# Kernel tuning notes

Hardware: AMD Instinct MI355X
Metric: run time of the kernel (lower is better)

Reference implementation:

```python
import jax, jax.numpy as jnp
import numpy as np

N_NODES = 100000
N_EDGES = 1600000
HIDDEN = 128
IN_CH = 128


def setup_inputs() -> dict:
    key = jax.random.key(0)
    ks = jax.random.split(key, 7)
    x = jax.random.normal(ks[0], (N_NODES, IN_CH), dtype=jnp.float32)
    # edge_index with no self-loops (col != row), matching remove_self_loops
    row = jax.random.randint(ks[1], (N_EDGES,), 0, N_NODES)
    off = jax.random.randint(ks[2], (N_EDGES,), 1, N_NODES)
    col = (row + off) % N_NODES
    edge_index = jnp.stack([row, col], axis=0).astype(jnp.int64)
    Wi = jax.random.normal(ks[3], (HIDDEN, IN_CH), dtype=jnp.float32) * (1.0 / np.sqrt(IN_CH))
    bi = jax.random.normal(ks[4], (HIDDEN,), dtype=jnp.float32) * 0.01
    A = jax.random.normal(ks[5], (HIDDEN, HIDDEN), dtype=jnp.float32) * (1.0 / np.sqrt(HIDDEN))
    Wp = jax.random.normal(ks[6], (HIDDEN, HIDDEN + 2), dtype=jnp.float32) * (1.0 / np.sqrt(HIDDEN))
    return {"x": x, "edge_index": edge_index, "Wi": Wi, "bi": bi, "A": A,
            "Wp": Wp, "num_layers": 4}


def _pairwise_weight(Wp):
    # W0: strictly-upper part symmetrized; diag = q * row-abs-sum + r
    W0 = jnp.triu(Wp[:, :-2], 1)
    W0 = W0 + W0.T
    q = Wp[:, -2]
    r = Wp[:, -1]
    return W0 + jnp.diag(q * jnp.sum(jnp.abs(W0), axis=1) + r)


def reference(x, edge_index, Wi, bi, A, Wp, num_layers):
    n = x.shape[0]
    row, col = edge_index[0], edge_index[1]
    # degree-based symmetric normalization (degree of target nodes)
    deg = jax.ops.segment_sum(jnp.ones_like(col, dtype=x.dtype), col, num_segments=n)
    dinv = jnp.where(deg > 0, jax.lax.rsqrt(jnp.maximum(deg, 1.0)), 0.0)
    norm = dinv[row] * dinv[col]  # [edges]

    Weff = _pairwise_weight(Wp)          # symmetric [H, H]
    Asym = A - A.T                       # antisymmetric [H, H]

    h = jax.nn.relu(x @ Wi.T + bi)       # input projection (dropout eval = id)
    for _ in range(num_layers):
        out = h @ Weff.T                 # symmetric aggr pre-mix
        msg = norm[:, None] * out[row]   # gather + per-edge scale [E, H]
        agg = jax.ops.segment_sum(msg, col, num_segments=n)  # scatter-add
        delta = agg - jax.nn.relu(h @ Asym.T)
        h = h + jax.nn.relu(jnp.tanh(delta))
    return h
```

## Files before the change

kernel.cpp:

```cpp
#include <hip/hip_runtime.h>
#include <hip/hip_bf16.h>

#define HID 128
#define NLAYERS 4
#define SCHUNK 2048
#define WSHIFT 13

typedef __attribute__((ext_vector_type(8))) short bf16x8;
typedef __attribute__((ext_vector_type(4))) float f32x4;

__device__ __forceinline__ float bf2f(unsigned short u) {
    union { unsigned int i; float f; } v; v.i = ((unsigned int)u) << 16; return v.f;
}
__device__ __forceinline__ unsigned short f2bf(float f) {
    union { float f; unsigned int i; } v; v.f = f;
    unsigned int r = v.i + 0x7FFF + ((v.i >> 16) & 1);
    return (unsigned short)(r >> 16);
}

__global__ void k_detect(const unsigned int* ei, int* flag) {
    __shared__ int s;
    if (threadIdx.x == 0) s = 1;
    __syncthreads();
    unsigned int w = ei[threadIdx.x * 2 + 1];
    if (w != 0) s = 0;
    __syncthreads();
    if (threadIdx.x == 0) *flag = s;
}

__global__ void k_convert_edges(const void* ei, const int* flag, int* row32, int* col32,
                                int* deg, int ne) {
    int e = blockIdx.x * blockDim.x + threadIdx.x;
    if (e >= ne) return;
    int r, c;
    if (*flag) {
        const long long* p = (const long long*)ei;
        r = (int)p[e];
        c = (int)p[(size_t)ne + e];
    } else {
        const int* p = (const int*)ei;
        r = p[e];
        c = p[(size_t)ne + e];
    }
    row32[e] = r;
    col32[e] = c;
    atomicAdd(&deg[c], 1);
}

__global__ void k_scan1(const int* deg, int* partial, float* dinv, int n) {
    int tid = threadIdx.x, lane = tid & 63, wid = tid >> 6;
    int i0 = blockIdx.x * SCHUNK + tid * 8;
    int ts = 0;
    #pragma unroll
    for (int j = 0; j < 8; ++j) {
        int i = i0 + j;
        if (i < n) {
            int d = deg[i];
            ts += d;
            dinv[i] = (d > 0) ? rsqrtf((float)d) : 0.f;
        }
    }
    #pragma unroll
    for (int m = 1; m < 64; m <<= 1) ts += __shfl_xor(ts, m);
    __shared__ int ws[4];
    if (lane == 0) ws[wid] = ts;
    __syncthreads();
    if (tid == 0) partial[blockIdx.x] = ws[0] + ws[1] + ws[2] + ws[3];
}

__global__ void k_scan2(int* partial, int nb) {
    int tid = threadIdx.x;
    int v = (tid < nb) ? partial[tid] : 0;
    int s = v;
    #pragma unroll
    for (int off = 1; off < 64; off <<= 1) {
        int t = __shfl_up(s, off);
        if (tid >= off) s += t;
    }
    if (tid < nb) partial[tid] = s - v;
}

__global__ void k_scan3(const int* deg, const int* partial, int* offs, int* pos, int n, int ne) {
    int tid = threadIdx.x, lane = tid & 63, wid = tid >> 6;
    int i0 = blockIdx.x * SCHUNK + tid * 8;
    int v[8], ts = 0;
    #pragma unroll
    for (int j = 0; j < 8; ++j) { v[j] = (i0 + j < n) ? deg[i0 + j] : 0; ts += v[j]; }
    int s = ts;
    #pragma unroll
    for (int off = 1; off < 64; off <<= 1) { int t = __shfl_up(s, off); if (lane >= off) s += t; }
    __shared__ int ws[4];
    if (lane == 63) ws[wid] = s;
    __syncthreads();
    int run = partial[blockIdx.x] + (s - ts);
    for (int w = 0; w < wid; ++w) run += ws[w];
    #pragma unroll
    for (int j = 0; j < 8; ++j) {
        if (i0 + j < n) { offs[i0 + j] = run; pos[i0 + j] = run; }
        run += v[j];
    }
    if (blockIdx.x == 0 && tid == 0) offs[n] = ne;
}

__global__ void k_csrfill(const int* row32, const int* col32, int* pos, int* csr,
                          int ne, int nwin) {
    int cls = blockIdx.x & 7;
    int slice = blockIdx.x >> 3;
    int e0 = (slice * blockDim.x + threadIdx.x) * 4;
    int r[4], c[4], w[4];
    #pragma unroll
    for (int k = 0; k < 4; ++k) {
        int e = e0 + k;
        if (e < ne) { c[k] = col32[e]; r[k] = row32[e]; w[k] = c[k] >> WSHIFT; }
        else w[k] = -1;
    }
    for (int p = cls; p < nwin; p += 8) {
        #pragma unroll
        for (int k = 0; k < 4; ++k) {
            if (w[k] == p) {
                int q = atomicAdd(&pos[c[k]], 1);
                csr[q] = r[k];
            }
        }
    }
}

__global__ void k_weff(const float* Wp, unsigned short* WeffB) {
    int i = blockIdx.x, j = threadIdx.x;
    float w = (i < j) ? Wp[i * 130 + j] : ((i > j) ? Wp[j * 130 + i] : 0.f);
    float a = fabsf(w);
    #pragma unroll
    for (int m = 1; m < 64; m <<= 1) a += __shfl_xor(a, m);
    __shared__ float ws[2];
    if ((j & 63) == 0) ws[j >> 6] = a;
    __syncthreads();
    float rs = ws[0] + ws[1];
    if (i == j) w = Wp[i * 130 + 128] * rs + Wp[i * 130 + 129];
    WeffB[i * 128 + j] = f2bf(w);
}

__global__ void k_asym_wi(const float* A, const float* Wi, unsigned short* AsymB, unsigned short* WiB) {
    int idx = blockIdx.x * blockDim.x + threadIdx.x;
    if (idx >= 16384) return;
    int i = idx >> 7, j = idx & 127;
    AsymB[idx] = f2bf(A[idx] - A[j * 128 + i]);
    WiB[idx] = f2bf(Wi[idx]);
}

__launch_bounds__(256, 2)
__global__ void k_gemm0(const float* x, const unsigned short* WiB, const float* bi,
                        const float* dinv, float* h, unsigned short* hsb, int n) {
    int wid = threadIdx.x >> 6, lane = threadIdx.x & 63;
    int row0 = blockIdx.x * 64 + wid * 16;
    int lrow = lane & 15, lk = (lane >> 4) * 8;
    int arow = row0 + lrow; if (arow >= n) arow = n - 1;
    const float* Aptr = x + (size_t)arow * 128;
    f32x4 acc[8];
    #pragma unroll
    for (int cf = 0; cf < 8; ++cf) acc[cf] = (f32x4)(0.f);
    #pragma unroll
    for (int kk = 0; kk < 4; ++kk) {
        float4 xa = *(const float4*)(Aptr + kk * 32 + lk);
        float4 xc = *(const float4*)(Aptr + kk * 32 + lk + 4);
        bf16x8 a;
        a[0] = (short)f2bf(xa.x); a[1] = (short)f2bf(xa.y);
        a[2] = (short)f2bf(xa.z); a[3] = (short)f2bf(xa.w);
        a[4] = (short)f2bf(xc.x); a[5] = (short)f2bf(xc.y);
        a[6] = (short)f2bf(xc.z); a[7] = (short)f2bf(xc.w);
        #pragma unroll
        for (int cf = 0; cf < 8; ++cf) {
            bf16x8 b = *(const bf16x8*)(WiB + (size_t)(cf * 16 + lrow) * 128 + kk * 32 + lk);
            acc[cf] = __builtin_amdgcn_mfma_f32_16x16x32_bf16(a, b, acc[cf], 0, 0, 0);
        }
    }
    int orow_base = row0 + (lane >> 4) * 4;
    #pragma unroll
    for (int r = 0; r < 4; ++r) {
        int orow = orow_base + r;
        if (orow >= n) continue;
        float dv = dinv[orow];
        #pragma unroll
        for (int cf = 0; cf < 8; ++cf) {
            int col = cf * 16 + lrow;
            float v = acc[cf][r] + bi[col];
            v = fmaxf(v, 0.f);
            h[(size_t)orow * 128 + col] = v;
            hsb[(size_t)orow * 128 + col] = f2bf(v * dv);
        }
    }
}

__launch_bounds__(256, 8)
__global__ void k_gather(const unsigned short* hsb, const int* csr, const int* offs,
                         unsigned short* aggHb, int n) {
    int wid = threadIdx.x >> 6, lane = threadIdx.x & 63;
    int c = blockIdx.x * 4 + wid;
    if (c >= n) return;
    int g = lane >> 4;
    int fl = lane & 15;
    int s = offs[c], e = offs[c + 1];
    float accA[8], accB[8];
    #pragma unroll
    for (int k = 0; k < 8; ++k) { accA[k] = 0.f; accB[k] = 0.f; }
    int j = s;
    for (; j + 16 <= e; j += 16) {
        int r0 = csr[j + g];
        int r1 = csr[j + 4 + g];
        int r2 = csr[j + 8 + g];
        int r3 = csr[j + 12 + g];
        uint4 v0 = *(const uint4*)(hsb + (size_t)r0 * 128 + fl * 8);
        uint4 v1 = *(const uint4*)(hsb + (size_t)r1 * 128 + fl * 8);
        uint4 v2 = *(const uint4*)(hsb + (size_t)r2 * 128 + fl * 8);
        uint4 v3 = *(const uint4*)(hsb + (size_t)r3 * 128 + fl * 8);
        accA[0] += bf2f((unsigned short)(v0.x & 0xffff)); accA[1] += bf2f((unsigned short)(v0.x >> 16));
        accA[2] += bf2f((unsigned short)(v0.y & 0xffff)); accA[3] += bf2f((unsigned short)(v0.y >> 16));
        accA[4] += bf2f((unsigned short)(v0.z & 0xffff)); accA[5] += bf2f((unsigned short)(v0.z >> 16));
        accA[6] += bf2f((unsigned short)(v0.w & 0xffff)); accA[7] += bf2f((unsigned short)(v0.w >> 16));
        accB[0] += bf2f((unsigned short)(v1.x & 0xffff)); accB[1] += bf2f((unsigned short)(v1.x >> 16));
        accB[2] += bf2f((unsigned short)(v1.y & 0xffff)); accB[3] += bf2f((unsigned short)(v1.y >> 16));
        accB[4] += bf2f((unsigned short)(v1.z & 0xffff)); accB[5] += bf2f((unsigned short)(v1.z >> 16));
        accB[6] += bf2f((unsigned short)(v1.w & 0xffff)); accB[7] += bf2f((unsigned short)(v1.w >> 16));
        accA[0] += bf2f((unsigned short)(v2.x & 0xffff)); accA[1] += bf2f((unsigned short)(v2.x >> 16));
        accA[2] += bf2f((unsigned short)(v2.y & 0xffff)); accA[3] += bf2f((unsigned short)(v2.y >> 16));
        accA[4] += bf2f((unsigned short)(v2.z & 0xffff)); accA[5] += bf2f((unsigned short)(v2.z >> 16));
        accA[6] += bf2f((unsigned short)(v2.w & 0xffff)); accA[7] += bf2f((unsigned short)(v2.w >> 16));
        accB[0] += bf2f((unsigned short)(v3.x & 0xffff)); accB[1] += bf2f((unsigned short)(v3.x >> 16));
        accB[2] += bf2f((unsigned short)(v3.y & 0xffff)); accB[3] += bf2f((unsigned short)(v3.y >> 16));
        accB[4] += bf2f((unsigned short)(v3.z & 0xffff)); accB[5] += bf2f((unsigned short)(v3.z >> 16));
        accB[6] += bf2f((unsigned short)(v3.w & 0xffff)); accB[7] += bf2f((unsigned short)(v3.w >> 16));
    }
    for (; j < e; j += 8) {
        int i0 = j + g, i1 = j + 4 + g;
        if (i0 < e) {
            int r = csr[i0];
            uint4 v = *(const uint4*)(hsb + (size_t)r * 128 + fl * 8);
            accA[0] += bf2f((unsigned short)(v.x & 0xffff)); accA[1] += bf2f((unsigned short)(v.x >> 16));
            accA[2] += bf2f((unsigned short)(v.y & 0xffff)); accA[3] += bf2f((unsigned short)(v.y >> 16));
            accA[4] += bf2f((unsigned short)(v.z & 0xffff)); accA[5] += bf2f((unsigned short)(v.z >> 16));
            accA[6] += bf2f((unsigned short)(v.w & 0xffff)); accA[7] += bf2f((unsigned short)(v.w >> 16));
        }
        if (i1 < e) {
            int r = csr[i1];
            uint4 v = *(const uint4*)(hsb + (size_t)r * 128 + fl * 8);
            accB[0] += bf2f((unsigned short)(v.x & 0xffff)); accB[1] += bf2f((unsigned short)(v.x >> 16));
            accB[2] += bf2f((unsigned short)(v.y & 0xffff)); accB[3] += bf2f((unsigned short)(v.y >> 16));
            accB[4] += bf2f((unsigned short)(v.z & 0xffff)); accB[5] += bf2f((unsigned short)(v.z >> 16));
            accB[6] += bf2f((unsigned short)(v.w & 0xffff)); accB[7] += bf2f((unsigned short)(v.w >> 16));
        }
    }
    #pragma unroll
    for (int k = 0; k < 8; ++k) {
        float a = accA[k] + accB[k];
        a += __shfl_xor(a, 16);
        a += __shfl_xor(a, 32);
        accA[k] = a;
    }
    int f0 = fl * 8 + g * 2;
    unsigned int o = ((unsigned int)f2bf(accA[g * 2 + 1]) << 16) | (unsigned int)f2bf(accA[g * 2]);
    *(unsigned int*)(aggHb + (size_t)c * 128 + f0) = o;
}

__launch_bounds__(256, 8)
__global__ void k_gemm_upd(const unsigned short* aggHb, const unsigned short* WeffB,
                           const unsigned short* AsymB, const float* dinv,
                           float* h, unsigned short* hsb, int n) {
    __shared__ float zl[32][132];
    int wv = threadIdx.x >> 6, lane = threadIdx.x & 63;
    int t = wv & 1;
    int m = wv >> 1;
    int row0 = blockIdx.x * 32 + t * 16;
    int lrow = lane & 15, lk = (lane >> 4) * 8;
    int arow = row0 + lrow; if (arow >= n) arow = n - 1;
    f32x4 acc[8];
    #pragma unroll
    for (int cf = 0; cf < 8; ++cf) acc[cf] = (f32x4)(0.f);
    if (m == 1) {
        const float* Ap = h + (size_t)arow * 128;
        #pragma unroll
        for (int kk = 0; kk < 4; ++kk) {
            float4 xa = *(const float4*)(Ap + kk * 32 + lk);
            float4 xc = *(const float4*)(Ap + kk * 32 + lk + 4);
            bf16x8 a;
            a[0] = (short)f2bf(xa.x); a[1] = (short)f2bf(xa.y);
            a[2] = (short)f2bf(xa.z); a[3] = (short)f2bf(xa.w);
            a[4] = (short)f2bf(xc.x); a[5] = (short)f2bf(xc.y);
            a[6] = (short)f2bf(xc.z); a[7] = (short)f2bf(xc.w);
            #pragma unroll
            for (int cf = 0; cf < 8; ++cf) {
                bf16x8 b = *(const bf16x8*)(AsymB + (size_t)(cf * 16 + lrow) * 128 + kk * 32 + lk);
                acc[cf] = __builtin_amdgcn_mfma_f32_16x16x32_bf16(a, b, acc[cf], 0, 0, 0);
            }
        }
        int lr0 = t * 16 + (lane >> 4) * 4;
        #pragma unroll
        for (int r = 0; r < 4; ++r)
            #pragma unroll
            for (int cf = 0; cf < 8; ++cf)
                zl[lr0 + r][cf * 16 + lrow] = fmaxf(acc[cf][r], 0.f);
    } else {
        const bf16x8* Ap = (const bf16x8*)(aggHb + (size_t)arow * 128);
        #pragma unroll
        for (int kk = 0; kk < 4; ++kk) {
            bf16x8 a = Ap[kk * 4 + (lk >> 3)];
            #pragma unroll
            for (int cf = 0; cf < 8; ++cf) {
                bf16x8 b = *(const bf16x8*)(WeffB + (size_t)(cf * 16 + lrow) * 128 + kk * 32 + lk);
                acc[cf] = __builtin_amdgcn_mfma_f32_16x16x32_bf16(a, b, acc[cf], 0, 0, 0);
            }
        }
    }
    __syncthreads();
    if (m == 0) {
        int orow_base = row0 + (lane >> 4) * 4;
        int lr0 = t * 16 + (lane >> 4) * 4;
        #pragma unroll
        for (int r = 0; r < 4; ++r) {
            int orow = orow_base + r;
            if (orow >= n) continue;
            float dv = dinv[orow];
            #pragma unroll
            for (int cf = 0; cf < 8; ++cf) {
                int col = cf * 16 + lrow;
                float delta = dv * acc[cf][r] - zl[lr0 + r][col];
                float u = fmaxf(tanhf(delta), 0.f);
                size_t idx = (size_t)orow * 128 + col;
                float hv = h[idx] + u;
                h[idx] = hv;
                hsb[idx] = f2bf(hv * dv);
            }
        }
    }
}

extern "C" void kernel_launch(void* const* d_in, const int* in_sizes, int n_in,
                              void* d_out, int out_size, void* d_ws, size_t ws_size,
                              hipStream_t stream) {
    const float* x  = (const float*)d_in[0];
    const void*  ei = d_in[1];
    const float* Wi = (const float*)d_in[2];
    const float* bi = (const float*)d_in[3];
    const float* A  = (const float*)d_in[4];
    const float* Wp = (const float*)d_in[5];

    const int n  = in_sizes[0] / HID;
    const int ne = in_sizes[1] / 2;

    char* w = (char*)d_ws;
    size_t o = 0;
    auto alloc = [&](size_t bytes) -> void* {
        void* p = w + o;
        o = (o + bytes + 255) & ~(size_t)255;
        return p;
    };
    int*            flag    = (int*)alloc(4);
    int*            row32   = (int*)alloc((size_t)ne * 4);
    int*            col32   = (int*)alloc((size_t)ne * 4);
    int*            deg     = (int*)alloc((size_t)n * 4);
    float*          dinv    = (float*)alloc((size_t)n * 4);
    int*            offs    = (int*)alloc((size_t)(n + 1) * 4);
    int*            pos     = (int*)alloc((size_t)n * 4);
    int*            partial = (int*)alloc(64 * 4);
    int*            csr     = (int*)alloc((size_t)ne * 4);
    unsigned short* WeffB   = (unsigned short*)alloc(16384 * 2);
    unsigned short* AsymB   = (unsigned short*)alloc(16384 * 2);
    unsigned short* WiB     = (unsigned short*)alloc(16384 * 2);
    unsigned short* hsb     = (unsigned short*)alloc((size_t)n * 128 * 2);
    unsigned short* aggHb   = (unsigned short*)alloc((size_t)n * 128 * 2);
    if (o > ws_size) return;

    float* h = (float*)d_out;

    hipMemsetAsync(deg, 0, (size_t)n * 4, stream);

    int eb = (ne + 255) / 256;
    int sb = (n + SCHUNK - 1) / SCHUNK;
    int nwin = (n + (1 << WSHIFT) - 1) >> WSHIFT;

    k_detect<<<1, 256, 0, stream>>>((const unsigned int*)ei, flag);
    k_convert_edges<<<eb, 256, 0, stream>>>(ei, flag, row32, col32, deg, ne);
    k_scan1<<<sb, 256, 0, stream>>>(deg, partial, dinv, n);
    k_scan2<<<1, 64, 0, stream>>>(partial, sb);
    k_scan3<<<sb, 256, 0, stream>>>(deg, partial, offs, pos, n, ne);
    int fb = (ne + 1023) / 1024;
    k_csrfill<<<fb * 8, 256, 0, stream>>>(row32, col32, pos, csr, ne, nwin);
    k_weff<<<128, 128, 0, stream>>>(Wp, WeffB);
    k_asym_wi<<<64, 256, 0, stream>>>(A, Wi, AsymB, WiB);

    int gb = (n + 63) / 64;
    k_gemm0<<<gb, 256, 0, stream>>>(x, WiB, bi, dinv, h, hsb, n);

    int ab = (n + 3) / 4;
    int ub = (n + 31) / 32;
    for (int l = 0; l < NLAYERS; ++l) {
        k_gather<<<ab, 256, 0, stream>>>(hsb, csr, offs, aggHb, n);
        k_gemm_upd<<<ub, 256, 0, stream>>>(aggHb, WeffB, AsymB, dinv, h, hsb, n);
    }
}
```

Before: 814.8 us.

## Fuse neighbor gather into per-layer GEMM update kernel with ping-pong buffers

```diff
diff --git a/kernel.cpp b/kernel.cpp
--- a/kernel.cpp
+++ b/kernel.cpp
@@ -190,82 +190,84 @@
     }
 }
 
-__launch_bounds__(256, 8)
-__global__ void k_gather(const unsigned short* hsb, const int* csr, const int* offs,
-                         unsigned short* aggHb, int n) {
-    int wid = threadIdx.x >> 6, lane = threadIdx.x & 63;
-    int c = blockIdx.x * 4 + wid;
-    if (c >= n) return;
+__launch_bounds__(256, 6)
+__global__ void k_layer(const unsigned short* hsc, unsigned short* hsn,
+                        const int* csr, const int* offs,
+                        const unsigned short* WeffB, const unsigned short* AsymB,
+                        const float* dinv, float* h, int n) {
+    __shared__ unsigned short aggL[32][136];
+    __shared__ float zl[32][132];
+    int wv = threadIdx.x >> 6, lane = threadIdx.x & 63;
     int g = lane >> 4;
     int fl = lane & 15;
-    int s = offs[c], e = offs[c + 1];
-    float accA[8], accB[8];
-    #pragma unroll
-    for (int k = 0; k < 8; ++k) { accA[k] = 0.f; accB[k] = 0.f; }
-    int j = s;
-    for (; j + 16 <= e; j += 16) {
-        int r0 = csr[j + g];
-        int r1 = csr[j + 4 + g];
-        int r2 = csr[j + 8 + g];
-        int r3 = csr[j + 12 + g];
-        uint4 v0 = *(const uint4*)(hsb + (size_t)r0 * 128 + fl * 8);
-        uint4 v1 = *(const uint4*)(hsb + (size_t)r1 * 128 + fl * 8);
-        uint4 v2 = *(const uint4*)(hsb + (size_t)r2 * 128 + fl * 8);
-        uint4 v3 = *(const uint4*)(hsb + (size_t)r3 * 128 + fl * 8);
-        accA[0] += bf2f((unsigned short)(v0.x & 0xffff)); accA[1] += bf2f((unsigned short)(v0.x >> 16));
-        accA[2] += bf2f((unsigned short)(v0.y & 0xffff)); accA[3] += bf2f((unsigned short)(v0.y >> 16));
-        accA[4] += bf2f((unsigned short)(v0.z & 0xffff)); accA[5] += bf2f((unsigned short)(v0.z >> 16));
-        accA[6] += bf2f((unsigned short)(v0.w & 0xffff)); accA[7] += bf2f((unsigned short)(v0.w >> 16));
-        accB[0] += bf2f((unsigned short)(v1.x & 0xffff)); accB[1] += bf2f((unsigned short)(v1.x >> 16));
-        accB[2] += bf2f((unsigned short)(v1.y & 0xffff)); accB[3] += bf2f((unsigned short)(v1.y >> 16));
-        accB[4] += bf2f((unsigned short)(v1.z & 0xffff)); accB[5] += bf2f((unsigned short)(v1.z >> 16));
-        accB[6] += bf2f((unsigned short)(v1.w & 0xffff)); accB[7] += bf2f((unsigned short)(v1.w >> 16));
-        accA[0] += bf2f((unsigned short)(v2.x & 0xffff)); accA[1] += bf2f((unsigned short)(v2.x >> 16));
-        accA[2] += bf2f((unsigned short)(v2.y & 0xffff)); accA[3] += bf2f((unsigned short)(v2.y >> 16));
-        accA[4] += bf2f((unsigned short)(v2.z & 0xffff)); accA[5] += bf2f((unsigned short)(v2.z >> 16));
-        accA[6] += bf2f((unsigned short)(v2.w & 0xffff)); accA[7] += bf2f((unsigned short)(v2.w >> 16));
-        accB[0] += bf2f((unsigned short)(v3.x & 0xffff)); accB[1] += bf2f((unsigned short)(v3.x >> 16));
-        accB[2] += bf2f((unsigned short)(v3.y & 0xffff)); accB[3] += bf2f((unsigned short)(v3.y >> 16));
-        accB[4] += bf2f((unsigned short)(v3.z & 0xffff)); accB[5] += bf2f((unsigned short)(v3.z >> 16));
-        accB[6] += bf2f((unsigned short)(v3.w & 0xffff)); accB[7] += bf2f((unsigned short)(v3.w >> 16));
-    }
-    for (; j < e; j += 8) {
-        int i0 = j + g, i1 = j + 4 + g;
-        if (i0 < e) {
-            int r = csr[i0];
-            uint4 v = *(const uint4*)(hsb + (size_t)r * 128 + fl * 8);
-            accA[0] += bf2f((unsigned short)(v.x & 0xffff)); accA[1] += bf2f((unsigned short)(v.x >> 16));
-            accA[2] += bf2f((unsigned short)(v.y & 0xffff)); accA[3] += bf2f((unsigned short)(v.y >> 16));
-            accA[4] += bf2f((unsigned short)(v.z & 0xffff)); accA[5] += bf2f((unsigned short)(v.z >> 16));
-            accA[6] += bf2f((unsigned short)(v.w & 0xffff)); accA[7] += bf2f((unsigned short)(v.w >> 16));
-        }
-        if (i1 < e) {
-            int r = csr[i1];
-            uint4 v = *(const uint4*)(hsb + (size_t)r * 128 + fl * 8);
-            accB[0] += bf2f((unsigned short)(v.x & 0xffff)); accB[1] += bf2f((unsigned short)(v.x >> 16));
-            accB[2] += bf2f((unsigned short)(v.y & 0xffff)); accB[3] += bf2f((unsigned short)(v.y >> 16));
-            accB[4] += bf2f((unsigned short)(v.z & 0xffff)); accB[5] += bf2f((unsigned short)(v.z >> 16));
-            accB[6] += bf2f((unsigned short)(v.w & 0xffff)); accB[7] += bf2f((unsigned short)(v.w >> 16));
-        }
-    }
-    #pragma unroll
-    for (int k = 0; k < 8; ++k) {
-        float a = accA[k] + accB[k];
-        a += __shfl_xor(a, 16);
-        a += __shfl_xor(a, 32);
-        accA[k] = a;
-    }
-    int f0 = fl * 8 + g * 2;
-    unsigned int o = ((unsigned int)f2bf(accA[g * 2 + 1]) << 16) | (unsigned int)f2bf(accA[g * 2]);
-    *(unsigned int*)(aggHb + (size_t)c * 128 + f0) = o;
-}
-
-__launch_bounds__(256, 8)
-__global__ void k_gemm_upd(const unsigned short* aggHb, const unsigned short* WeffB,
-                           const unsigned short* AsymB, const float* dinv,
-                           float* h, unsigned short* hsb, int n) {
-    __shared__ float zl[32][132];
-    int wv = threadIdx.x >> 6, lane = threadIdx.x & 63;
+
+    int cbase = blockIdx.x * 32 + wv * 8;
+    for (int q = 0; q < 8; ++q) {
+        int c = cbase + q;
+        if (c >= n) break;
+        int s = offs[c], e = offs[c + 1];
+        float accA[8], accB[8];
+        #pragma unroll
+        for (int k = 0; k < 8; ++k) { accA[k] = 0.f; accB[k] = 0.f; }
+        int j = s;
+        for (; j + 16 <= e; j += 16) {
+            int r0 = csr[j + g];
+            int r1 = csr[j + 4 + g];
+            int r2 = csr[j + 8 + g];
+            int r3 = csr[j + 12 + g];
+            uint4 v0 = *(const uint4*)(hsc + (size_t)r0 * 128 + fl * 8);
+            uint4 v1 = *(const uint4*)(hsc + (size_t)r1 * 128 + fl * 8);
+            uint4 v2 = *(const uint4*)(hsc + (size_t)r2 * 128 + fl * 8);
+            uint4 v3 = *(const uint4*)(hsc + (size_t)r3 * 128 + fl * 8);
+            accA[0] += bf2f((unsigned short)(v0.x & 0xffff)); accA[1] += bf2f((unsigned short)(v0.x >> 16));
+            accA[2] += bf2f((unsigned short)(v0.y & 0xffff)); accA[3] += bf2f((unsigned short)(v0.y >> 16));
+            accA[4] += bf2f((unsigned short)(v0.z & 0xffff)); accA[5] += bf2f((unsigned short)(v0.z >> 16));
+            accA[6] += bf2f((unsigned short)(v0.w & 0xffff)); accA[7] += bf2f((unsigned short)(v0.w >> 16));
+            accB[0] += bf2f((unsigned short)(v1.x & 0xffff)); accB[1] += bf2f((unsigned short)(v1.x >> 16));
+            accB[2] += bf2f((unsigned short)(v1.y & 0xffff)); accB[3] += bf2f((unsigned short)(v1.y >> 16));
+            accB[4] += bf2f((unsigned short)(v1.z & 0xffff)); accB[5] += bf2f((unsigned short)(v1.z >> 16));
+            accB[6] += bf2f((unsigned short)(v1.w & 0xffff)); accB[7] += bf2f((unsigned short)(v1.w >> 16));
+            accA[0] += bf2f((unsigned short)(v2.x & 0xffff)); accA[1] += bf2f((unsigned short)(v2.x >> 16));
+            accA[2] += bf2f((unsigned short)(v2.y & 0xffff)); accA[3] += bf2f((unsigned short)(v2.y >> 16));
+            accA[4] += bf2f((unsigned short)(v2.z & 0xffff)); accA[5] += bf2f((unsigned short)(v2.z >> 16));
+            accA[6] += bf2f((unsigned short)(v2.w & 0xffff)); accA[7] += bf2f((unsigned short)(v2.w >> 16));
+            accB[0] += bf2f((unsigned short)(v3.x & 0xffff)); accB[1] += bf2f((unsigned short)(v3.x >> 16));
+            accB[2] += bf2f((unsigned short)(v3.y & 0xffff)); accB[3] += bf2f((unsigned short)(v3.y >> 16));
+            accB[4] += bf2f((unsigned short)(v3.z & 0xffff)); accB[5] += bf2f((unsigned short)(v3.z >> 16));
+            accB[6] += bf2f((unsigned short)(v3.w & 0xffff)); accB[7] += bf2f((unsigned short)(v3.w >> 16));
+        }
+        for (; j < e; j += 8) {
+            int i0 = j + g, i1 = j + 4 + g;
+            if (i0 < e) {
+                int r = csr[i0];
+                uint4 v = *(const uint4*)(hsc + (size_t)r * 128 + fl * 8);
+                accA[0] += bf2f((unsigned short)(v.x & 0xffff)); accA[1] += bf2f((unsigned short)(v.x >> 16));
+                accA[2] += bf2f((unsigned short)(v.y & 0xffff)); accA[3] += bf2f((unsigned short)(v.y >> 16));
+                accA[4] += bf2f((unsigned short)(v.z & 0xffff)); accA[5] += bf2f((unsigned short)(v.z >> 16));
+                accA[6] += bf2f((unsigned short)(v.w & 0xffff)); accA[7] += bf2f((unsigned short)(v.w >> 16));
+            }
+            if (i1 < e) {
+                int r = csr[i1];
+                uint4 v = *(const uint4*)(hsc + (size_t)r * 128 + fl * 8);
+                accB[0] += bf2f((unsigned short)(v.x & 0xffff)); accB[1] += bf2f((unsigned short)(v.x >> 16));
+                accB[2] += bf2f((unsigned short)(v.y & 0xffff)); accB[3] += bf2f((unsigned short)(v.y >> 16));
+                accB[4] += bf2f((unsigned short)(v.z & 0xffff)); accB[5] += bf2f((unsigned short)(v.z >> 16));
+                accB[6] += bf2f((unsigned short)(v.w & 0xffff)); accB[7] += bf2f((unsigned short)(v.w >> 16));
+            }
+        }
+        #pragma unroll
+        for (int k = 0; k < 8; ++k) {
+            float a = accA[k] + accB[k];
+            a += __shfl_xor(a, 16);
+            a += __shfl_xor(a, 32);
+            accA[k] = a;
+        }
+        int f0 = fl * 8 + g * 2;
+        unsigned int o = ((unsigned int)f2bf(accA[g * 2 + 1]) << 16) | (unsigned int)f2bf(accA[g * 2]);
+        *(unsigned int*)&aggL[wv * 8 + q][f0] = o;
+    }
+    __syncthreads();
+
     int t = wv & 1;
     int m = wv >> 1;
     int row0 = blockIdx.x * 32 + t * 16;
@@ -298,10 +300,9 @@
             for (int cf = 0; cf < 8; ++cf)
                 zl[lr0 + r][cf * 16 + lrow] = fmaxf(acc[cf][r], 0.f);
     } else {
-        const bf16x8* Ap = (const bf16x8*)(aggHb + (size_t)arow * 128);
         #pragma unroll
         for (int kk = 0; kk < 4; ++kk) {
-            bf16x8 a = Ap[kk * 4 + (lk >> 3)];
+            bf16x8 a = *(const bf16x8*)&aggL[t * 16 + lrow][kk * 32 + lk];
             #pragma unroll
             for (int cf = 0; cf < 8; ++cf) {
                 bf16x8 b = *(const bf16x8*)(WeffB + (size_t)(cf * 16 + lrow) * 128 + kk * 32 + lk);
@@ -326,7 +327,7 @@
                 size_t idx = (size_t)orow * 128 + col;
                 float hv = h[idx] + u;
                 h[idx] = hv;
-                hsb[idx] = f2bf(hv * dv);
+                hsn[idx] = f2bf(hv * dv);
             }
         }
     }
@@ -364,8 +365,8 @@
     unsigned short* WeffB   = (unsigned short*)alloc(16384 * 2);
     unsigned short* AsymB   = (unsigned short*)alloc(16384 * 2);
     unsigned short* WiB     = (unsigned short*)alloc(16384 * 2);
-    unsigned short* hsb     = (unsigned short*)alloc((size_t)n * 128 * 2);
-    unsigned short* aggHb   = (unsigned short*)alloc((size_t)n * 128 * 2);
+    unsigned short* hsA     = (unsigned short*)alloc((size_t)n * 128 * 2);
+    unsigned short* hsB     = (unsigned short*)alloc((size_t)n * 128 * 2);
     if (o > ws_size) return;
 
     float* h = (float*)d_out;
@@ -387,12 +388,12 @@
     k_asym_wi<<<64, 256, 0, stream>>>(A, Wi, AsymB, WiB);
 
     int gb = (n + 63) / 64;
-    k_gemm0<<<gb, 256, 0, stream>>>(x, WiB, bi, dinv, h, hsb, n);
-
-    int ab = (n + 3) / 4;
+    k_gemm0<<<gb, 256, 0, stream>>>(x, WiB, bi, dinv, h, hsA, n);
+
     int ub = (n + 31) / 32;
     for (int l = 0; l < NLAYERS; ++l) {
-        k_gather<<<ab, 256, 0, stream>>>(hsb, csr, offs, aggHb, n);
-        k_gemm_upd<<<ub, 256, 0, stream>>>(aggHb, WeffB, AsymB, dinv, h, hsb, n);
-    }
-}
+        unsigned short* cur = (l & 1) ? hsB : hsA;
+        unsigned short* nxt = (l & 1) ? hsA : hsB;
+        k_layer<<<ub, 256, 0, stream>>>(cur, nxt, csr, offs, WeffB, AsymB, dinv, h, n);
+    }
+}
```

After: 819.3 us. No clear change (+0.6%).
